# Kernel optimization log

Measured on AMD Instinct MI355X. Metric: run time of the kernel, lower is better.

The kernel has to match this reference:

```python
import jax, jax.numpy as jnp
import numpy as np

NEG_SLOPE = 0.2  # PyG GATv2Conv default negative_slope


def gatv2_layer(x, src, dst, edge_attr, Wl, bl, Wr, br, We, att, bias, n_nodes):
    """Faithful PyG GATv2Conv (concat=True, eval mode / no dropout).
    x: [N, Fin]; src/dst: [E]; edge_attr: [E, Fe]; att: [H, C].
    Returns [N, H*C].
    """
    H, C = att.shape
    xl = (x @ Wl + bl).reshape(-1, H, C)        # source-side transform (x_j)
    xr = (x @ Wr + br).reshape(-1, H, C)        # target-side transform (x_i)
    e_emb = (edge_attr @ We).reshape(-1, H, C)
    # per-edge pre-activation: x_i + x_j + edge
    g = jax.nn.leaky_relu(xl[src] + xr[dst] + e_emb, NEG_SLOPE)  # [E, H, C]
    logits = jnp.einsum('ehc,hc->eh', g, att)                    # [E, H]
    # segment softmax grouped by destination node
    m = jax.ops.segment_max(logits, dst, num_segments=n_nodes)   # [N, H]
    m = jnp.where(jnp.isfinite(m), m, 0.0)                       # empty segments
    a = jnp.exp(logits - m[dst])
    denom = jax.ops.segment_sum(a, dst, num_segments=n_nodes)    # [N, H]
    alpha = a / (denom[dst] + 1e-16)
    msg = xl[src] * alpha[:, :, None]                            # [E, H, C]
    out = jax.ops.segment_sum(msg, dst, num_segments=n_nodes)    # [N, H, C]
    return out.reshape(n_nodes, H * C) + bias


def setup_inputs() -> dict:
    key = jax.random.key(0)
    ks = jax.random.split(key, 24)
    N, E = 100000, 1600000
    Fin, Hd, Fe = 6, 64, 2
    g = lambda k, shp: (jax.random.normal(k, shp, dtype=jnp.float32) * 0.1)
    inp = {
        'x': jax.random.normal(ks[0], (N, Fin), dtype=jnp.float32),
        'edge_index': jax.random.randint(ks[1], (2, E), 0, N, dtype=jnp.int32),
        'edge_attr': jax.random.normal(ks[2], (E, Fe), dtype=jnp.float32),
        # layer 1: heads=2, out=64 -> H*C = 128
        'Wl1': g(ks[3], (Fin, 128)), 'bl1': jnp.zeros((128,), jnp.float32),
        'Wr1': g(ks[4], (Fin, 128)), 'br1': jnp.zeros((128,), jnp.float32),
        'We1': g(ks[5], (Fe, 128)),
        'att1': g(ks[6], (2, Hd)),
        'bias1': jnp.zeros((128,), jnp.float32),
        # layer 2: heads=1, in=128, out=64
        'Wl2': g(ks[7], (128, Hd)), 'bl2': jnp.zeros((Hd,), jnp.float32),
        'Wr2': g(ks[8], (128, Hd)), 'br2': jnp.zeros((Hd,), jnp.float32),
        'We2': g(ks[9], (Fe, Hd)),
        'att2': g(ks[10], (1, Hd)),
        'bias2': jnp.zeros((Hd,), jnp.float32),
        # MLP head
        'Wh1': g(ks[11], (Hd, Hd)), 'bh1': jnp.zeros((Hd,), jnp.float32),
        'Wh2': g(ks[12], (Hd, 1)), 'bh2': jnp.zeros((1,), jnp.float32),
    }
    return inp


def reference(x, edge_index, edge_attr,
              Wl1, bl1, Wr1, br1, We1, att1, bias1,
              Wl2, bl2, Wr2, br2, We2, att2, bias2,
              Wh1, bh1, Wh2, bh2):
    N = x.shape[0]
    src, dst = edge_index[0], edge_index[1]
    h = gatv2_layer(x, src, dst, edge_attr, Wl1, bl1, Wr1, br1, We1, att1, bias1, N)
    h = jax.nn.relu(h)
    h = gatv2_layer(h, src, dst, edge_attr, Wl2, bl2, Wr2, br2, We2, att2, bias2, N)
    h = jax.nn.relu(h)
    out = jax.nn.relu(h @ Wh1 + bh1) @ Wh2 + bh2  # [N, 1]
    return out[:, 0]
```

## Files before the change

kernel.cpp:

```cpp
#include <hip/hip_runtime.h>
#include <hip/hip_bf16.h>

#define NEG_SLOPE 0.2f
#define LOG2E 1.44269504088896f

#define NB_SHIFT 9
#define NB_NODES 512
#define NBLK_PART 256

typedef _Float16 half8 __attribute__((ext_vector_type(8)));
typedef _Float16 half4 __attribute__((ext_vector_type(4)));
typedef _Float16 half2t __attribute__((ext_vector_type(2)));

__device__ __forceinline__ void ld4(float* d, const float* p) {
    float4 t = *(const float4*)p;
    d[0] = t.x; d[1] = t.y; d[2] = t.z; d[3] = t.w;
}

__device__ __forceinline__ unsigned pack2h(float a, float b) {
    union { half2t h; unsigned u; } pk;
    pk.h[0] = (_Float16)a; pk.h[1] = (_Float16)b;
    return pk.u;
}

__device__ __forceinline__ half2t u2h2(unsigned u) {
    union { unsigned u; half2t h; } c; c.u = u; return c.h;
}
__device__ __forceinline__ half2t f2h2(float a, float b) {
    half2t r; r[0] = (_Float16)a; r[1] = (_Float16)b; return r;
}

#if __has_builtin(__builtin_amdgcn_perm)
#define PERMB(a, b, s) __builtin_amdgcn_perm((a), (b), (s))
#else
__device__ __forceinline__ unsigned PERMB(unsigned a, unsigned b, unsigned s) {
    unsigned long long v = ((unsigned long long)a << 32) | b;
    unsigned r = 0;
#pragma unroll
    for (int i = 0; i < 4; ++i) {
        unsigned idx = (s >> (8 * i)) & 0xFF;
        r |= ((unsigned)(v >> (8 * idx)) & 0xFF) << (8 * i);
    }
    return r;
}
#endif

#if __has_builtin(__builtin_amdgcn_fdot2)
#define FDOT2(a, b, c) __builtin_amdgcn_fdot2((a), (b), (c), false)
#else
#define FDOT2(a, b, c) fmaf((float)(a)[1], (float)(b)[1], fmaf((float)(a)[0], (float)(b)[0], (c)))
#endif

#define DPP_ADD(x, ctrl) \
    ((x) + __int_as_float(__builtin_amdgcn_update_dpp(0, __float_as_int(x), (ctrl), 0xf, 0xf, true)))
#define ROW_REDUCE16(x) do { \
    x = DPP_ADD(x, 0x128); \
    x = DPP_ADD(x, 0x124); \
    x = DPP_ADD(x, 0x122); \
    x = DPP_ADD(x, 0x121); \
} while (0)

#define CHGRP(xl2, xr2, wa, wb, at2, ex, ey, logit) do { \
    half2t z_ = (xl2) + (xr2); \
    z_ = __builtin_elementwise_fma((ex), (wa), z_); \
    z_ = __builtin_elementwise_fma((ey), (wb), z_); \
    z_ = __builtin_elementwise_max(z_, z_ * NEGS); \
    logit = FDOT2(z_, (at2), logit); \
} while (0)

__global__ void __launch_bounds__(256) prep_kernel(
    const float* __restrict__ x,
    const float* __restrict__ Wl1, const float* __restrict__ bl1,
    const float* __restrict__ Wr1, const float* __restrict__ br1,
    _Float16* __restrict__ xlh, _Float16* __restrict__ xrh, int N)
{
    int gt = blockIdx.x * blockDim.x + threadIdx.x;
    int n = gt >> 6, c = gt & 63;
    if (n >= N) return;
    const float* xrow = x + (size_t)n * 6;
    float l0 = bl1[c], l1 = bl1[64 + c];
    float r0 = br1[c], r1 = br1[64 + c];
#pragma unroll
    for (int f = 0; f < 6; ++f) {
        float xv = xrow[f];
        l0 = fmaf(xv, Wl1[f * 128 + c], l0);
        l1 = fmaf(xv, Wl1[f * 128 + 64 + c], l1);
        r0 = fmaf(xv, Wr1[f * 128 + c], r0);
        r1 = fmaf(xv, Wr1[f * 128 + 64 + c], r1);
    }
    *(unsigned*)(xlh + (size_t)n * 128 + 2 * c) = pack2h(l0, l1);
    *(unsigned*)(xrh + (size_t)n * 128 + 2 * c) = pack2h(r0, r1);
}

__global__ void __launch_bounds__(256) partA_count(
    const int* __restrict__ dstv, int* __restrict__ M, int E, int EPB, int NB)
{
    __shared__ int hist[256];
    int blk = blockIdx.x, t = threadIdx.x;
    if (t < NB) hist[t] = 0;
    __syncthreads();
    int s0 = blk * EPB;
    int s1 = min(s0 + EPB, E);
    for (int e = s0 + t; e < s1; e += 256)
        atomicAdd(&hist[((unsigned)dstv[e]) >> NB_SHIFT], 1);
    __syncthreads();
    if (t < NB) M[t * NBLK_PART + blk] = hist[t];
}

__global__ void __launch_bounds__(256) partB1_scanrow(
    int* __restrict__ M, int* __restrict__ btot)
{
    __shared__ int lds[256];
    int bkt = blockIdx.x, t = threadIdx.x;
    int cnt = M[bkt * NBLK_PART + t];
    lds[t] = cnt;
    __syncthreads();
    for (int s = 1; s < 256; s <<= 1) {
        int v = (t >= s) ? lds[t - s] : 0;
        __syncthreads();
        lds[t] += v;
        __syncthreads();
    }
    M[bkt * NBLK_PART + t] = lds[t] - cnt;
    if (t == 255) btot[bkt] = lds[255];
}

__global__ void partB2_scanbkt(const int* __restrict__ btot, int* __restrict__ boff,
                               int* __restrict__ off, int NB, int N, int E)
{
    if (threadIdx.x == 0) {
        int run = 0;
        for (int i = 0; i < NB; ++i) { boff[i] = run; run += btot[i]; }
        boff[NB] = run;
        off[N] = E;
    }
}

__global__ void __launch_bounds__(256) partC_scatter(
    const int* __restrict__ srcv, const int* __restrict__ dstv,
    const float2* __restrict__ ea2, const int* __restrict__ M,
    const int* __restrict__ boff,
    int2* __restrict__ ebuf, int* __restrict__ dbuf,
    int E, int EPB, int NB)
{
    __shared__ int cur[256];
    int blk = blockIdx.x, t = threadIdx.x;
    if (t < NB) cur[t] = M[t * NBLK_PART + blk] + boff[t];
    __syncthreads();
    int s0 = blk * EPB;
    int s1 = min(s0 + EPB, E);
    for (int e = s0 + t; e < s1; e += 256) {
        int d = dstv[e];
        int bkt = ((unsigned)d) >> NB_SHIFT;
        int p = atomicAdd(&cur[bkt], 1);
        float2 ea = ea2[e];
        int2 v; v.x = srcv[e]; v.y = (int)pack2h(ea.x, ea.y);
        ebuf[p] = v;
        dbuf[p] = d;
    }
}

__global__ void __launch_bounds__(256) partD_finalize(
    const int2* __restrict__ ebuf, const int* __restrict__ dbuf,
    const int* __restrict__ boff,
    int* __restrict__ off, int2* __restrict__ csr_edge, int N)
{
    __shared__ int hist[NB_NODES];
    int b = blockIdx.x, t = threadIdx.x;
    int node_base = b << NB_SHIFT;
    int nnodes = min(NB_NODES, N - node_base);
    int seg_s = boff[b], seg_e = boff[b + 1];
    for (int i = t; i < NB_NODES; i += 256) hist[i] = 0;
    __syncthreads();
    for (int e = seg_s + t; e < seg_e; e += 256)
        atomicAdd(&hist[dbuf[e] - node_base], 1);
    __syncthreads();
    if (t == 0) {
        int run = 0;
        for (int i = 0; i < nnodes; ++i) { int c = hist[i]; hist[i] = run; run += c; }
    }
    __syncthreads();
    for (int i = t; i < nnodes; i += 256) off[node_base + i] = seg_s + hist[i];
    __syncthreads();
    for (int e = seg_s + t; e < seg_e; e += 256) {
        int dl = dbuf[e] - node_base;
        int r = atomicAdd(&hist[dl], 1);
        csr_edge[seg_s + r] = ebuf[e];
    }
}

__global__ void __launch_bounds__(256) c1_kernel(
    const int* __restrict__ off, const int2* __restrict__ csr_edge,
    const _Float16* __restrict__ xlh, const _Float16* __restrict__ xrh,
    const float* __restrict__ We1, const float* __restrict__ att1,
    const float* __restrict__ bias1,
    _Float16* __restrict__ h1h, int N)
{
    int wv = (blockIdx.x * blockDim.x + threadIdx.x) >> 6;
    int lane = threadIdx.x & 63;
    if (2 * wv >= N) return;
    int half = lane >> 5;
    int n = 2 * wv + half;
    bool nvalid = (n < N);
    int nc = nvalid ? n : 0;
    int l = lane & 31;
    int g = l & 15;
    int slot = (l >> 4) & 1;
    unsigned gb = (unsigned)(g << 4);

    const half2t NEGS = f2h2(NEG_SLOPE, NEG_SLOPE);

    half2t a0h[2], a1h[2], w00h[2], w01h[2], w10h[2], w11h[2];
    {
        float t[4];
        ld4(t, att1 + 4 * g);
        a0h[0] = f2h2(t[0] * LOG2E, t[1] * LOG2E); a0h[1] = f2h2(t[2] * LOG2E, t[3] * LOG2E);
        ld4(t, att1 + 64 + 4 * g);
        a1h[0] = f2h2(t[0] * LOG2E, t[1] * LOG2E); a1h[1] = f2h2(t[2] * LOG2E, t[3] * LOG2E);
        ld4(t, We1 + 4 * g);        w00h[0] = f2h2(t[0], t[1]); w00h[1] = f2h2(t[2], t[3]);
        ld4(t, We1 + 64 + 4 * g);   w01h[0] = f2h2(t[0], t[1]); w01h[1] = f2h2(t[2], t[3]);
        ld4(t, We1 + 128 + 4 * g);  w10h[0] = f2h2(t[0], t[1]); w10h[1] = f2h2(t[2], t[3]);
        ld4(t, We1 + 192 + 4 * g);  w11h[0] = f2h2(t[0], t[1]); w11h[1] = f2h2(t[2], t[3]);
    }

    half2t xr00, xr01, xr10, xr11;
    {
        half8 xrv = *(const half8*)(xrh + (size_t)nc * 128 + 8 * g);
        xr00[0] = xrv[0]; xr00[1] = xrv[2];
        xr01[0] = xrv[4]; xr01[1] = xrv[6];
        xr10[0] = xrv[1]; xr10[1] = xrv[3];
        xr11[0] = xrv[5]; xr11[1] = xrv[7];
    }

    int s = off[nc];
    int e = nvalid ? off[nc + 1] : s;
    int m = e - s;
    int mo = __shfl_xor(m, 32);
    int iters = (max(m, mo) + 3) >> 2;

    float a0A[4] = {0,0,0,0}, a1A[4] = {0,0,0,0};
    float a0B[4] = {0,0,0,0}, a1B[4] = {0,0,0,0};
    float d0A = 0.f, d1A = 0.f, d0B = 0.f, d1B = 0.f;

    const char* xlb = (const char*)xlh;

    int pA0 = s + slot, pB0 = s + 2 + slot;
    bool vA0 = (pA0 < e), vB0 = (pB0 < e);
    int2 edA0 = csr_edge[vA0 ? pA0 : 0];
    int2 edB0 = csr_edge[vB0 ? pB0 : 0];
    int pA1 = s + 4 + slot, pB1 = s + 6 + slot;
    bool vA1 = (pA1 < e), vB1 = (pB1 < e);
    int2 edA1 = csr_edge[vA1 ? pA1 : 0];
    int2 edB1 = csr_edge[vB1 ? pB1 : 0];
    half8 hvA = *(const half8*)(xlb + (((unsigned)edA0.x) << 8) + gb);
    half8 hvB = *(const half8*)(xlb + (((unsigned)edB0.x) << 8) + gb);

    int p0 = s;
    for (int it = 0; it < iters; ++it, p0 += 4) {
        int pA2 = p0 + 8 + slot, pB2 = p0 + 10 + slot;
        bool vA2 = (pA2 < e), vB2 = (pB2 < e);
        int2 edA2 = csr_edge[vA2 ? pA2 : 0];
        int2 edB2 = csr_edge[vB2 ? pB2 : 0];

        half8 hvAn = *(const half8*)(xlb + (((unsigned)edA1.x) << 8) + gb);
        half8 hvBn = *(const half8*)(xlb + (((unsigned)edB1.x) << 8) + gb);

        unsigned uA = (unsigned)edA0.y, uB = (unsigned)edB0.y;
        half2t exA = u2h2(PERMB(uA, uA, 0x01000100));
        half2t eyA = u2h2(PERMB(uA, uA, 0x03020302));
        half2t exB = u2h2(PERMB(uB, uB, 0x01000100));
        half2t eyB = u2h2(PERMB(uB, uB, 0x03020302));

        union { half8 h; unsigned u[4]; } HA, HB;
        HA.h = hvA; HB.h = hvB;
        half2t xA00 = u2h2(PERMB(HA.u[1], HA.u[0], 0x05040100));
        half2t xA01 = u2h2(PERMB(HA.u[3], HA.u[2], 0x05040100));
        half2t xA10 = u2h2(PERMB(HA.u[1], HA.u[0], 0x07060302));
        half2t xA11 = u2h2(PERMB(HA.u[3], HA.u[2], 0x07060302));
        half2t xB00 = u2h2(PERMB(HB.u[1], HB.u[0], 0x05040100));
        half2t xB01 = u2h2(PERMB(HB.u[3], HB.u[2], 0x05040100));
        half2t xB10 = u2h2(PERMB(HB.u[1], HB.u[0], 0x07060302));
        half2t xB11 = u2h2(PERMB(HB.u[3], HB.u[2], 0x07060302));

        float pA0f = 0.f, pA1f = 0.f, pB0f = 0.f, pB1f = 0.f;
        CHGRP(xA00, xr00, w00h[0], w10h[0], a0h[0], exA, eyA, pA0f);
        CHGRP(xA01, xr01, w00h[1], w10h[1], a0h[1], exA, eyA, pA0f);
        CHGRP(xA10, xr10, w01h[0], w11h[0], a1h[0], exA, eyA, pA1f);
        CHGRP(xA11, xr11, w01h[1], w11h[1], a1h[1], exA, eyA, pA1f);
        CHGRP(xB00, xr00, w00h[0], w10h[0], a0h[0], exB, eyB, pB0f);
        CHGRP(xB01, xr01, w00h[1], w10h[1], a0h[1], exB, eyB, pB0f);
        CHGRP(xB10, xr10, w01h[0], w11h[0], a1h[0], exB, eyB, pB1f);
        CHGRP(xB11, xr11, w01h[1], w11h[1], a1h[1], exB, eyB, pB1f);

        ROW_REDUCE16(pA0f);
        ROW_REDUCE16(pA1f);
        ROW_REDUCE16(pB0f);
        ROW_REDUCE16(pB1f);

        float eA0 = vA0 ? exp2f(pA0f) : 0.f;
        float eA1 = vA0 ? exp2f(pA1f) : 0.f;
        float eB0 = vB0 ? exp2f(pB0f) : 0.f;
        float eB1 = vB0 ? exp2f(pB1f) : 0.f;
        d0A += eA0; d1A += eA1;
        d0B += eB0; d1B += eB1;

        a0A[0] = fmaf(eA0, (float)hvA[0], a0A[0]);
        a0A[1] = fmaf(eA0, (float)hvA[2], a0A[1]);
        a0A[2] = fmaf(eA0, (float)hvA[4], a0A[2]);
        a0A[3] = fmaf(eA0, (float)hvA[6], a0A[3]);
        a1A[0] = fmaf(eA1, (float)hvA[1], a1A[0]);
        a1A[1] = fmaf(eA1, (float)hvA[3], a1A[1]);
        a1A[2] = fmaf(eA1, (float)hvA[5], a1A[2]);
        a1A[3] = fmaf(eA1, (float)hvA[7], a1A[3]);
        a0B[0] = fmaf(eB0, (float)hvB[0], a0B[0]);
        a0B[1] = fmaf(eB0, (float)hvB[2], a0B[1]);
        a0B[2] = fmaf(eB0, (float)hvB[4], a0B[2]);
        a0B[3] = fmaf(eB0, (float)hvB[6], a0B[3]);
        a1B[0] = fmaf(eB1, (float)hvB[1], a1B[0]);
        a1B[1] = fmaf(eB1, (float)hvB[3], a1B[1]);
        a1B[2] = fmaf(eB1, (float)hvB[5], a1B[2]);
        a1B[3] = fmaf(eB1, (float)hvB[7], a1B[3]);

        edA0 = edA1; edB0 = edB1; vA0 = vA1; vB0 = vB1;
        edA1 = edA2; edB1 = edB2; vA1 = vA2; vB1 = vB2;
        hvA = hvAn; hvB = hvBn;
    }

    float acc0[4], acc1[4];
#pragma unroll
    for (int i = 0; i < 4; ++i) { acc0[i] = a0A[i] + a0B[i]; acc1[i] = a1A[i] + a1B[i]; }
    float d0 = d0A + d0B, d1 = d1A + d1B;
#pragma unroll
    for (int i = 0; i < 4; ++i) {
        acc0[i] += __shfl_xor(acc0[i], 16);
        acc1[i] += __shfl_xor(acc1[i], 16);
    }
    d0 += __shfl_xor(d0, 16);
    d1 += __shfl_xor(d1, 16);

    if (slot == 0 && nvalid) {
        float b0[4], b1[4];
        ld4(b0, bias1 + 4 * g);
        ld4(b1, bias1 + 64 + 4 * g);
        float r0 = 1.f / (d0 + 1e-16f), r1 = 1.f / (d1 + 1e-16f);
        half4 o0, o1;
        o0[0] = (_Float16)fmaxf(fmaf(acc0[0], r0, b0[0]), 0.f);
        o0[1] = (_Float16)fmaxf(fmaf(acc0[1], r0, b0[1]), 0.f);
        o0[2] = (_Float16)fmaxf(fmaf(acc0[2], r0, b0[2]), 0.f);
        o0[3] = (_Float16)fmaxf(fmaf(acc0[3], r0, b0[3]), 0.f);
        o1[0] = (_Float16)fmaxf(fmaf(acc1[0], r1, b1[0]), 0.f);
        o1[1] = (_Float16)fmaxf(fmaf(acc1[1], r1, b1[1]), 0.f);
        o1[2] = (_Float16)fmaxf(fmaf(acc1[2], r1, b1[2]), 0.f);
        o1[3] = (_Float16)fmaxf(fmaf(acc1[3], r1, b1[3]), 0.f);
        *(half4*)(h1h + (size_t)n * 128 + 4 * g) = o0;
        *(half4*)(h1h + (size_t)n * 128 + 64 + 4 * g) = o1;
    }
}

__global__ void __launch_bounds__(256) a2_kernel(
    const _Float16* __restrict__ h1h,
    const float* __restrict__ Wl2, const float* __restrict__ bl2,
    const float* __restrict__ Wr2, const float* __restrict__ br2,
    _Float16* __restrict__ xl2h, _Float16* __restrict__ xr2h, int N)
{
    __shared__ float hs[64 * 128];
    int tid = threadIdx.x;
    int n0 = blockIdx.x * 64;

    for (int i = tid; i < 64 * 16; i += 256) {
        int row = i >> 4;
        int q = i & 15;
        int n = n0 + row;
        float f[8];
        if (n < N) {
            half8 v = *(const half8*)(h1h + (size_t)n * 128 + q * 8);
#pragma unroll
            for (int j = 0; j < 8; ++j) f[j] = (float)v[j];
        } else {
#pragma unroll
            for (int j = 0; j < 8; ++j) f[j] = 0.f;
        }
        *(float4*)(hs + row * 128 + q * 8)     = make_float4(f[0], f[1], f[2], f[3]);
        *(float4*)(hs + row * 128 + q * 8 + 4) = make_float4(f[4], f[5], f[6], f[7]);
    }
    __syncthreads();

    int cslot = tid & 31;
    int jgrp = tid >> 5;
    int c4 = cslot * 4;
    bool isL = (c4 < 64);
    int cc = isL ? c4 : (c4 - 64);
    const float* Wb = (isL ? Wl2 : Wr2) + cc;
    const float* bb = (isL ? bl2 : br2) + cc;
    float4 bias = *(const float4*)bb;

    float acc[8][4];
#pragma unroll
    for (int j = 0; j < 8; ++j) {
        acc[j][0] = bias.x; acc[j][1] = bias.y;
        acc[j][2] = bias.z; acc[j][3] = bias.w;
    }

    const float* hrow = hs + (jgrp * 8) * 128;
#pragma unroll 2
    for (int k4 = 0; k4 < 32; ++k4) {
        float4 w0 = *(const float4*)(Wb + (4 * k4 + 0) * 64);
        float4 w1 = *(const float4*)(Wb + (4 * k4 + 1) * 64);
        float4 w2 = *(const float4*)(Wb + (4 * k4 + 2) * 64);
        float4 w3 = *(const float4*)(Wb + (4 * k4 + 3) * 64);
#pragma unroll
        for (int j = 0; j < 8; ++j) {
            float4 hv = *(const float4*)(hrow + j * 128 + k4 * 4);
            acc[j][0] = fmaf(hv.x, w0.x, acc[j][0]);
            acc[j][1] = fmaf(hv.x, w0.y, acc[j][1]);
            acc[j][2] = fmaf(hv.x, w0.z, acc[j][2]);
            acc[j][3] = fmaf(hv.x, w0.w, acc[j][3]);
            acc[j][0] = fmaf(hv.y, w1.x, acc[j][0]);
            acc[j][1] = fmaf(hv.y, w1.y, acc[j][1]);
            acc[j][2] = fmaf(hv.y, w1.z, acc[j][2]);
            acc[j][3] = fmaf(hv.y, w1.w, acc[j][3]);
            acc[j][0] = fmaf(hv.z, w2.x, acc[j][0]);
            acc[j][1] = fmaf(hv.z, w2.y, acc[j][1]);
            acc[j][2] = fmaf(hv.z, w2.z, acc[j][2]);
            acc[j][3] = fmaf(hv.z, w2.w, acc[j][3]);
            acc[j][0] = fmaf(hv.w, w3.x, acc[j][0]);
            acc[j][1] = fmaf(hv.w, w3.y, acc[j][1]);
            acc[j][2] = fmaf(hv.w, w3.z, acc[j][2]);
            acc[j][3] = fmaf(hv.w, w3.w, acc[j][3]);
        }
    }

    _Float16* outb = isL ? xl2h : xr2h;
#pragma unroll
    for (int j = 0; j < 8; ++j) {
        int n = n0 + jgrp * 8 + j;
        if (n < N) {
            half4 o;
            o[0] = (_Float16)acc[j][0];
            o[1] = (_Float16)acc[j][1];
            o[2] = (_Float16)acc[j][2];
            o[3] = (_Float16)acc[j][3];
            *(half4*)(outb + (size_t)n * 64 + cc) = o;
        }
    }
}

__global__ void __launch_bounds__(256) c2_kernel(
    const int* __restrict__ off, const int2* __restrict__ csr_edge,
    const _Float16* __restrict__ xl2h, const _Float16* __restrict__ xr2h,
    const float* __restrict__ We2, const float* __restrict__ att2,
    const float* __restrict__ bias2,
    float* __restrict__ h2out, int N)
{
    int wv = (blockIdx.x * blockDim.x + threadIdx.x) >> 6;
    int lane = threadIdx.x & 63;
    if (2 * wv >= N) return;
    int half = lane >> 5;
    int n = 2 * wv + half;
    bool nvalid = (n < N);
    int nc = nvalid ? n : 0;
    int l = lane & 31;
    int g = l & 15;
    int slot = (l >> 4) & 1;
    unsigned gb = (unsigned)(g << 3);

    const half2t NEGS = f2h2(NEG_SLOPE, NEG_SLOPE);

    half2t avh[2], w0h[2], w1h[2], xr2[2];
    {
        float t[4];
        ld4(t, att2 + 4 * g);
        avh[0] = f2h2(t[0] * LOG2E, t[1] * LOG2E); avh[1] = f2h2(t[2] * LOG2E, t[3] * LOG2E);
        ld4(t, We2 + 4 * g);       w0h[0] = f2h2(t[0], t[1]); w0h[1] = f2h2(t[2], t[3]);
        ld4(t, We2 + 64 + 4 * g);  w1h[0] = f2h2(t[0], t[1]); w1h[1] = f2h2(t[2], t[3]);
        half4 xh = *(const half4*)(xr2h + (size_t)nc * 64 + 4 * g);
        xr2[0][0] = xh[0]; xr2[0][1] = xh[1];
        xr2[1][0] = xh[2]; xr2[1][1] = xh[3];
    }

    int s = off[nc];
    int e = nvalid ? off[nc + 1] : s;
    int m = e - s;
    int mo = __shfl_xor(m, 32);
    int iters = (max(m, mo) + 3) >> 2;

    float dA = 0.f, dB = 0.f;
    float aA[4] = {0,0,0,0}, aB[4] = {0,0,0,0};

    const char* xlb = (const char*)xl2h;

    int pA0 = s + slot, pB0 = s + 2 + slot;
    bool vA0 = (pA0 < e), vB0 = (pB0 < e);
    int2 edA0 = csr_edge[vA0 ? pA0 : 0];
    int2 edB0 = csr_edge[vB0 ? pB0 : 0];
    int pA1 = s + 4 + slot, pB1 = s + 6 + slot;
    bool vA1 = (pA1 < e), vB1 = (pB1 < e);
    int2 edA1 = csr_edge[vA1 ? pA1 : 0];
    int2 edB1 = csr_edge[vB1 ? pB1 : 0];
    half4 hvA = *(const half4*)(xlb + (((unsigned)edA0.x) << 7) + gb);
    half4 hvB = *(const half4*)(xlb + (((unsigned)edB0.x) << 7) + gb);

    int p0 = s;
    for (int it = 0; it < iters; ++it, p0 += 4) {
        int pA2 = p0 + 8 + slot, pB2 = p0 + 10 + slot;
        bool vA2 = (pA2 < e), vB2 = (pB2 < e);
        int2 edA2 = csr_edge[vA2 ? pA2 : 0];
        int2 edB2 = csr_edge[vB2 ? pB2 : 0];

        half4 hvAn = *(const half4*)(xlb + (((unsigned)edA1.x) << 7) + gb);
        half4 hvBn = *(const half4*)(xlb + (((unsigned)edB1.x) << 7) + gb);

        unsigned uA = (unsigned)edA0.y, uB = (unsigned)edB0.y;
        half2t exA = u2h2(PERMB(uA, uA, 0x01000100));
        half2t eyA = u2h2(PERMB(uA, uA, 0x03020302));
        half2t exB = u2h2(PERMB(uB, uB, 0x01000100));
        half2t eyB = u2h2(PERMB(uB, uB, 0x03020302));

        union { half4 h; unsigned u[2]; } HA, HB;
        HA.h = hvA; HB.h = hvB;
        half2t xA0 = u2h2(HA.u[0]), xA1 = u2h2(HA.u[1]);
        half2t xB0 = u2h2(HB.u[0]), xB1 = u2h2(HB.u[1]);

        float pA_ = 0.f, pB_ = 0.f;
        CHGRP(xA0, xr2[0], w0h[0], w1h[0], avh[0], exA, eyA, pA_);
        CHGRP(xA1, xr2[1], w0h[1], w1h[1], avh[1], exA, eyA, pA_);
        CHGRP(xB0, xr2[0], w0h[0], w1h[0], avh[0], exB, eyB, pB_);
        CHGRP(xB1, xr2[1], w0h[1], w1h[1], avh[1], exB, eyB, pB_);

        ROW_REDUCE16(pA_);
        ROW_REDUCE16(pB_);
        float evA = vA0 ? exp2f(pA_) : 0.f;
        float evB = vB0 ? exp2f(pB_) : 0.f;
        dA += evA; dB += evB;

        aA[0] = fmaf(evA, (float)hvA[0], aA[0]);
        aA[1] = fmaf(evA, (float)hvA[1], aA[1]);
        aA[2] = fmaf(evA, (float)hvA[2], aA[2]);
        aA[3] = fmaf(evA, (float)hvA[3], aA[3]);
        aB[0] = fmaf(evB, (float)hvB[0], aB[0]);
        aB[1] = fmaf(evB, (float)hvB[1], aB[1]);
        aB[2] = fmaf(evB, (float)hvB[2], aB[2]);
        aB[3] = fmaf(evB, (float)hvB[3], aB[3]);

        edA0 = edA1; edB0 = edB1; vA0 = vA1; vB0 = vB1;
        edA1 = edA2; edB1 = edB2; vA1 = vA2; vB1 = vB2;
        hvA = hvAn; hvB = hvBn;
    }

    float acc[4];
#pragma unroll
    for (int i = 0; i < 4; ++i) acc[i] = aA[i] + aB[i];
    float dsum = dA + dB;
#pragma unroll
    for (int i = 0; i < 4; ++i) acc[i] += __shfl_xor(acc[i], 16);
    dsum += __shfl_xor(dsum, 16);

    if (slot == 0 && nvalid) {
        float b2[4];
        ld4(b2, bias2 + 4 * g);
        float r = 1.f / (dsum + 1e-16f);
        float4 o;
        o.x = fmaxf(fmaf(acc[0], r, b2[0]), 0.f);
        o.y = fmaxf(fmaf(acc[1], r, b2[1]), 0.f);
        o.z = fmaxf(fmaf(acc[2], r, b2[2]), 0.f);
        o.w = fmaxf(fmaf(acc[3], r, b2[3]), 0.f);
        *(float4*)(h2out + (size_t)n * 64 + 4 * g) = o;
    }
}

__global__ void __launch_bounds__(256) head_kernel(
    const float* __restrict__ h2, const float* __restrict__ Wh1,
    const float* __restrict__ bh1, const float* __restrict__ Wh2,
    const float* __restrict__ bh2, float* __restrict__ out, int N)
{
    __shared__ float hs[64 * 68];
    int tid = threadIdx.x;
    int n0 = blockIdx.x * 64;

    for (int i = tid; i < 64 * 16; i += 256) {
        int row = i >> 4, q = i & 15;
        int n = n0 + row;
        float4 v = (n < N) ? *(const float4*)(h2 + (size_t)n * 64 + q * 4)
                           : make_float4(0.f, 0.f, 0.f, 0.f);
        *(float4*)(hs + row * 68 + q * 4) = v;
    }
    __syncthreads();

    int cslot = tid & 15;
    int jgrp  = tid >> 4;
    int c4 = cslot * 4;
    float4 bias = *(const float4*)(bh1 + c4);

    float acc[4][4];
#pragma unroll
    for (int r = 0; r < 4; ++r) {
        acc[r][0] = bias.x; acc[r][1] = bias.y;
        acc[r][2] = bias.z; acc[r][3] = bias.w;
    }

    const float* hrow = hs + (jgrp * 4) * 68;
#pragma unroll 2
    for (int k4 = 0; k4 < 16; ++k4) {
        float4 w0 = *(const float4*)(Wh1 + (4 * k4 + 0) * 64 + c4);
        float4 w1 = *(const float4*)(Wh1 + (4 * k4 + 1) * 64 + c4);
        float4 w2 = *(const float4*)(Wh1 + (4 * k4 + 2) * 64 + c4);
        float4 w3 = *(const float4*)(Wh1 + (4 * k4 + 3) * 64 + c4);
#pragma unroll
        for (int r = 0; r < 4; ++r) {
            float4 hv = *(const float4*)(hrow + r * 68 + k4 * 4);
            acc[r][0] = fmaf(hv.x, w0.x, acc[r][0]);
            acc[r][1] = fmaf(hv.x, w0.y, acc[r][1]);
            acc[r][2] = fmaf(hv.x, w0.z, acc[r][2]);
            acc[r][3] = fmaf(hv.x, w0.w, acc[r][3]);
            acc[r][0] = fmaf(hv.y, w1.x, acc[r][0]);
            acc[r][1] = fmaf(hv.y, w1.y, acc[r][1]);
            acc[r][2] = fmaf(hv.y, w1.z, acc[r][2]);
            acc[r][3] = fmaf(hv.y, w1.w, acc[r][3]);
            acc[r][0] = fmaf(hv.z, w2.x, acc[r][0]);
            acc[r][1] = fmaf(hv.z, w2.y, acc[r][1]);
            acc[r][2] = fmaf(hv.z, w2.z, acc[r][2]);
            acc[r][3] = fmaf(hv.z, w2.w, acc[r][3]);
            acc[r][0] = fmaf(hv.w, w3.x, acc[r][0]);
            acc[r][1] = fmaf(hv.w, w3.y, acc[r][1]);
            acc[r][2] = fmaf(hv.w, w3.z, acc[r][2]);
            acc[r][3] = fmaf(hv.w, w3.w, acc[r][3]);
        }
    }

    float4 w2v = *(const float4*)(Wh2 + c4);
    float p[4];
#pragma unroll
    for (int r = 0; r < 4; ++r) {
        p[r] = fmaxf(acc[r][0], 0.f) * w2v.x
             + fmaxf(acc[r][1], 0.f) * w2v.y
             + fmaxf(acc[r][2], 0.f) * w2v.z
             + fmaxf(acc[r][3], 0.f) * w2v.w;
    }
#pragma unroll
    for (int m = 1; m <= 8; m <<= 1) {
#pragma unroll
        for (int r = 0; r < 4; ++r) p[r] += __shfl_xor(p[r], m);
    }
    if (cslot == 0) {
        float b = bh2[0];
#pragma unroll
        for (int r = 0; r < 4; ++r) {
            int n = n0 + jgrp * 4 + r;
            if (n < N) out[n] = p[r] + b;
        }
    }
}

extern "C" void kernel_launch(void* const* d_in, const int* in_sizes, int n_in,
                              void* d_out, int out_size, void* d_ws, size_t ws_size,
                              hipStream_t stream) {
    const float* x    = (const float*)d_in[0];
    const int*   ei   = (const int*)d_in[1];
    const float* ea   = (const float*)d_in[2];
    const float* Wl1  = (const float*)d_in[3];
    const float* bl1  = (const float*)d_in[4];
    const float* Wr1  = (const float*)d_in[5];
    const float* br1  = (const float*)d_in[6];
    const float* We1  = (const float*)d_in[7];
    const float* att1 = (const float*)d_in[8];
    const float* bias1= (const float*)d_in[9];
    const float* Wl2  = (const float*)d_in[10];
    const float* bl2  = (const float*)d_in[11];
    const float* Wr2  = (const float*)d_in[12];
    const float* br2  = (const float*)d_in[13];
    const float* We2  = (const float*)d_in[14];
    const float* att2 = (const float*)d_in[15];
    const float* bias2= (const float*)d_in[16];
    const float* Wh1  = (const float*)d_in[17];
    const float* bh1  = (const float*)d_in[18];
    const float* Wh2  = (const float*)d_in[19];
    const float* bh2  = (const float*)d_in[20];

    int N = in_sizes[0] / 6;
    int E = in_sizes[1] / 2;
    const int* srcv = ei;
    const int* dstv = ei + E;

    int NB = (N + NB_NODES - 1) >> NB_SHIFT;
    int EPB = (E + NBLK_PART - 1) / NBLK_PART;

    char* w = (char*)d_ws;
    auto align256 = [](size_t v) { return (v + 255) & ~(size_t)255; };
    _Float16* xlh = (_Float16*)w;
    char* ip = w + align256((size_t)N * 128 * 2);
    _Float16* xrh = (_Float16*)ip; ip += align256((size_t)N * 128 * 2);
    _Float16* h1h = (_Float16*)ip; ip += align256((size_t)N * 128 * 2);
    _Float16* xl2h = (_Float16*)ip; ip += align256((size_t)N * 64 * 2);
    _Float16* xr2h = (_Float16*)ip; ip += align256((size_t)N * 64 * 2);
    int* off = (int*)ip;  ip += align256((size_t)(N + 1) * 4);
    int* Mbuf = (int*)ip; ip += align256((size_t)NB * NBLK_PART * 4);
    int* btot = (int*)ip; ip += align256((size_t)NB * 4);
    int* boff = (int*)ip; ip += align256((size_t)(NB + 1) * 4);
    int2* csr_edge = (int2*)ip;

    int2* ebuf = (int2*)h1h;
    int* dbuf = (int*)((char*)h1h + (size_t)E * 8);
    float* h2 = (float*)xlh;

    prep_kernel<<<((size_t)N * 64 + 255) / 256, 256, 0, stream>>>(
        x, Wl1, bl1, Wr1, br1, xlh, xrh, N);
    partA_count<<<NBLK_PART, 256, 0, stream>>>(dstv, Mbuf, E, EPB, NB);
    partB1_scanrow<<<NB, 256, 0, stream>>>(Mbuf, btot);
    partB2_scanbkt<<<1, 64, 0, stream>>>(btot, boff, off, NB, N, E);
    partC_scatter<<<NBLK_PART, 256, 0, stream>>>(
        srcv, dstv, (const float2*)ea, Mbuf, boff, ebuf, dbuf, E, EPB, NB);
    partD_finalize<<<NB, 256, 0, stream>>>(ebuf, dbuf, boff, off, csr_edge, N);
    size_t nwv = (size_t)((N + 1) / 2);
    c1_kernel<<<(nwv * 64 + 255) / 256, 256, 0, stream>>>(
        off, csr_edge, xlh, xrh, We1, att1, bias1, h1h, N);
    a2_kernel<<<(N + 63) / 64, 256, 0, stream>>>(
        h1h, Wl2, bl2, Wr2, br2, xl2h, xr2h, N);
    c2_kernel<<<(nwv * 64 + 255) / 256, 256, 0, stream>>>(
        off, csr_edge, xl2h, xr2h, We2, att2, bias2, h2, N);
    head_kernel<<<(N + 63) / 64, 256, 0, stream>>>(
        h2, Wh1, bh1, Wh2, bh2, (float*)d_out, N);
}
```

Measured before the change: 437.0 us.

## Pack local dst into src bits and pre-permute xl/xr fp16 layout

The scatter pass now packs the destination's low 9 bits into the upper bits of the source index, so the separate dbuf array is no longer written or read during CSR finalization. This removes one 4-byte-per-edge stream in both partitioning kernels. Separately, prep_kernel writes xl/xr in an interleaved order that matches the c1 consumer, so the per-edge byte permutes in the hot loop go away. The packing relies on node indices fitting in 23 bits, which holds for N=100000.

```diff
diff --git a/kernel.cpp b/kernel.cpp
--- a/kernel.cpp
+++ b/kernel.cpp
@@ -75,21 +75,25 @@
     _Float16* __restrict__ xlh, _Float16* __restrict__ xrh, int N)
 {
     int gt = blockIdx.x * blockDim.x + threadIdx.x;
-    int n = gt >> 6, c = gt & 63;
+    int n = gt >> 6, t = gt & 63;
     if (n >= N) return;
+    int h = t >> 5;
+    int cp = t & 31;
+    int c0 = h * 64 + 2 * cp;
     const float* xrow = x + (size_t)n * 6;
-    float l0 = bl1[c], l1 = bl1[64 + c];
-    float r0 = br1[c], r1 = br1[64 + c];
+    float la = bl1[c0], lb = bl1[c0 + 1];
+    float ra = br1[c0], rb = br1[c0 + 1];
 #pragma unroll
     for (int f = 0; f < 6; ++f) {
         float xv = xrow[f];
-        l0 = fmaf(xv, Wl1[f * 128 + c], l0);
-        l1 = fmaf(xv, Wl1[f * 128 + 64 + c], l1);
-        r0 = fmaf(xv, Wr1[f * 128 + c], r0);
-        r1 = fmaf(xv, Wr1[f * 128 + 64 + c], r1);
-    }
-    *(unsigned*)(xlh + (size_t)n * 128 + 2 * c) = pack2h(l0, l1);
-    *(unsigned*)(xrh + (size_t)n * 128 + 2 * c) = pack2h(r0, r1);
+        la = fmaf(xv, Wl1[f * 128 + c0], la);
+        lb = fmaf(xv, Wl1[f * 128 + c0 + 1], lb);
+        ra = fmaf(xv, Wr1[f * 128 + c0], ra);
+        rb = fmaf(xv, Wr1[f * 128 + c0 + 1], rb);
+    }
+    int pos = (cp >> 1) * 8 + h * 4 + (cp & 1) * 2;
+    *(unsigned*)(xlh + (size_t)n * 128 + pos) = pack2h(la, lb);
+    *(unsigned*)(xrh + (size_t)n * 128 + pos) = pack2h(ra, rb);
 }
 
 __global__ void __launch_bounds__(256) partA_count(
@@ -140,8 +144,7 @@
     const int* __restrict__ srcv, const int* __restrict__ dstv,
     const float2* __restrict__ ea2, const int* __restrict__ M,
     const int* __restrict__ boff,
-    int2* __restrict__ ebuf, int* __restrict__ dbuf,
-    int E, int EPB, int NB)
+    int2* __restrict__ ebuf, int E, int EPB, int NB)
 {
     __shared__ int cur[256];
     int blk = blockIdx.x, t = threadIdx.x;
@@ -154,15 +157,15 @@
         int bkt = ((unsigned)d) >> NB_SHIFT;
         int p = atomicAdd(&cur[bkt], 1);
         float2 ea = ea2[e];
-        int2 v; v.x = srcv[e]; v.y = (int)pack2h(ea.x, ea.y);
+        int2 v;
+        v.x = srcv[e] | ((d & (NB_NODES - 1)) << 23);
+        v.y = (int)pack2h(ea.x, ea.y);
         ebuf[p] = v;
-        dbuf[p] = d;
     }
 }
 
 __global__ void __launch_bounds__(256) partD_finalize(
-    const int2* __restrict__ ebuf, const int* __restrict__ dbuf,
-    const int* __restrict__ boff,
+    const int2* __restrict__ ebuf, const int* __restrict__ boff,
     int* __restrict__ off, int2* __restrict__ csr_edge, int N)
 {
     __shared__ int hist[NB_NODES];
@@ -173,7 +176,7 @@
     for (int i = t; i < NB_NODES; i += 256) hist[i] = 0;
     __syncthreads();
     for (int e = seg_s + t; e < seg_e; e += 256)
-        atomicAdd(&hist[dbuf[e] - node_base], 1);
+        atomicAdd(&hist[((unsigned)ebuf[e].x) >> 23], 1);
     __syncthreads();
     if (t == 0) {
         int run = 0;
@@ -183,9 +186,11 @@
     for (int i = t; i < nnodes; i += 256) off[node_base + i] = seg_s + hist[i];
     __syncthreads();
     for (int e = seg_s + t; e < seg_e; e += 256) {
-        int dl = dbuf[e] - node_base;
+        int2 v = ebuf[e];
+        int dl = ((unsigned)v.x) >> 23;
         int r = atomicAdd(&hist[dl], 1);
-        csr_edge[seg_s + r] = ebuf[e];
+        v.x &= 0x7FFFFF;
+        csr_edge[seg_s + r] = v;
     }
 }
 
@@ -226,10 +231,10 @@
     half2t xr00, xr01, xr10, xr11;
     {
         half8 xrv = *(const half8*)(xrh + (size_t)nc * 128 + 8 * g);
-        xr00[0] = xrv[0]; xr00[1] = xrv[2];
-        xr01[0] = xrv[4]; xr01[1] = xrv[6];
-        xr10[0] = xrv[1]; xr10[1] = xrv[3];
-        xr11[0] = xrv[5]; xr11[1] = xrv[7];
+        xr00[0] = xrv[0]; xr00[1] = xrv[1];
+        xr01[0] = xrv[2]; xr01[1] = xrv[3];
+        xr10[0] = xrv[4]; xr10[1] = xrv[5];
+        xr11[0] = xrv[6]; xr11[1] = xrv[7];
     }
 
     int s = off[nc];
@@ -273,14 +278,10 @@
 
         union { half8 h; unsigned u[4]; } HA, HB;
         HA.h = hvA; HB.h = hvB;
-        half2t xA00 = u2h2(PERMB(HA.u[1], HA.u[0], 0x05040100));
-        half2t xA01 = u2h2(PERMB(HA.u[3], HA.u[2], 0x05040100));
-        half2t xA10 = u2h2(PERMB(HA.u[1], HA.u[0], 0x07060302));
-        half2t xA11 = u2h2(PERMB(HA.u[3], HA.u[2], 0x07060302));
-        half2t xB00 = u2h2(PERMB(HB.u[1], HB.u[0], 0x05040100));
-        half2t xB01 = u2h2(PERMB(HB.u[3], HB.u[2], 0x05040100));
-        half2t xB10 = u2h2(PERMB(HB.u[1], HB.u[0], 0x07060302));
-        half2t xB11 = u2h2(PERMB(HB.u[3], HB.u[2], 0x07060302));
+        half2t xA00 = u2h2(HA.u[0]), xA01 = u2h2(HA.u[1]);
+        half2t xA10 = u2h2(HA.u[2]), xA11 = u2h2(HA.u[3]);
+        half2t xB00 = u2h2(HB.u[0]), xB01 = u2h2(HB.u[1]);
+        half2t xB10 = u2h2(HB.u[2]), xB11 = u2h2(HB.u[3]);
 
         float pA0f = 0.f, pA1f = 0.f, pB0f = 0.f, pB1f = 0.f;
         CHGRP(xA00, xr00, w00h[0], w10h[0], a0h[0], exA, eyA, pA0f);
@@ -305,20 +306,20 @@
         d0B += eB0; d1B += eB1;
 
         a0A[0] = fmaf(eA0, (float)hvA[0], a0A[0]);
-        a0A[1] = fmaf(eA0, (float)hvA[2], a0A[1]);
-        a0A[2] = fmaf(eA0, (float)hvA[4], a0A[2]);
-        a0A[3] = fmaf(eA0, (float)hvA[6], a0A[3]);
-        a1A[0] = fmaf(eA1, (float)hvA[1], a1A[0]);
-        a1A[1] = fmaf(eA1, (float)hvA[3], a1A[1]);
-        a1A[2] = fmaf(eA1, (float)hvA[5], a1A[2]);
+        a0A[1] = fmaf(eA0, (float)hvA[1], a0A[1]);
+        a0A[2] = fmaf(eA0, (float)hvA[2], a0A[2]);
+        a0A[3] = fmaf(eA0, (float)hvA[3], a0A[3]);
+        a1A[0] = fmaf(eA1, (float)hvA[4], a1A[0]);
+        a1A[1] = fmaf(eA1, (float)hvA[5], a1A[1]);
+        a1A[2] = fmaf(eA1, (float)hvA[6], a1A[2]);
         a1A[3] = fmaf(eA1, (float)hvA[7], a1A[3]);
         a0B[0] = fmaf(eB0, (float)hvB[0], a0B[0]);
-        a0B[1] = fmaf(eB0, (float)hvB[2], a0B[1]);
-        a0B[2] = fmaf(eB0, (float)hvB[4], a0B[2]);
-        a0B[3] = fmaf(eB0, (float)hvB[6], a0B[3]);
-        a1B[0] = fmaf(eB1, (float)hvB[1], a1B[0]);
-        a1B[1] = fmaf(eB1, (float)hvB[3], a1B[1]);
-        a1B[2] = fmaf(eB1, (float)hvB[5], a1B[2]);
+        a0B[1] = fmaf(eB0, (float)hvB[1], a0B[1]);
+        a0B[2] = fmaf(eB0, (float)hvB[2], a0B[2]);
+        a0B[3] = fmaf(eB0, (float)hvB[3], a0B[3]);
+        a1B[0] = fmaf(eB1, (float)hvB[4], a1B[0]);
+        a1B[1] = fmaf(eB1, (float)hvB[5], a1B[1]);
+        a1B[2] = fmaf(eB1, (float)hvB[6], a1B[2]);
         a1B[3] = fmaf(eB1, (float)hvB[7], a1B[3]);
 
         edA0 = edA1; edB0 = edB1; vA0 = vA1; vB0 = vB1;
@@ -699,7 +700,6 @@
     int2* csr_edge = (int2*)ip;
 
     int2* ebuf = (int2*)h1h;
-    int* dbuf = (int*)((char*)h1h + (size_t)E * 8);
     float* h2 = (float*)xlh;
 
     prep_kernel<<<((size_t)N * 64 + 255) / 256, 256, 0, stream>>>(
@@ -708,8 +708,8 @@
     partB1_scanrow<<<NB, 256, 0, stream>>>(Mbuf, btot);
     partB2_scanbkt<<<1, 64, 0, stream>>>(btot, boff, off, NB, N, E);
     partC_scatter<<<NBLK_PART, 256, 0, stream>>>(
-        srcv, dstv, (const float2*)ea, Mbuf, boff, ebuf, dbuf, E, EPB, NB);
-    partD_finalize<<<NB, 256, 0, stream>>>(ebuf, dbuf, boff, off, csr_edge, N);
+        srcv, dstv, (const float2*)ea, Mbuf, boff, ebuf, E, EPB, NB);
+    partD_finalize<<<NB, 256, 0, stream>>>(ebuf, boff, off, csr_edge, N);
     size_t nwv = (size_t)((N + 1) / 2);
     c1_kernel<<<(nwv * 64 + 255) / 256, 256, 0, stream>>>(
         off, csr_edge, xlh, xrh, We1, att1, bias1, h1h, N);
```

After: 438.8 us. No clear change (+0.4%).
